# Kernel optimization log

Measured on AMD Instinct MI355X. Metric: run time of the kernel, lower is better.

Reference implementation:

```python
import jax, jax.numpy as jnp
import numpy as np

CLAMP = 15  # relative positions clipped to [-15, 15], shifted to [0, 30]


def setup_inputs() -> dict:
    key = jax.random.key(0)
    ks = jax.random.split(key, 8)
    B, L, C, P = 2, 512, 256, 128
    return {
        "single_repr": jax.random.normal(ks[0], (B, L, C), jnp.float32),
        "pair_bias": jax.random.normal(ks[1], (B, L, L, 2), jnp.float32),
        "mask": jax.random.uniform(ks[2], (B, L), jnp.float32),
        "w_outer": jax.random.normal(ks[3], (C * C, P), jnp.float32) * (1.0 / C),
        "b_outer": jax.random.normal(ks[4], (P,), jnp.float32) * 0.02,
        "pos_embed": jax.random.normal(ks[5], (32, P), jnp.float32) * 0.02,
        "w_bias": jax.random.normal(ks[6], (2, P), jnp.float32) * 0.02,
        "b_bias": jax.random.normal(ks[7], (P,), jnp.float32) * 0.02,
    }


def reference(single_repr, pair_bias, mask, w_outer, b_outer, pos_embed, w_bias, b_bias):
    B, L, C = single_repr.shape
    P = w_outer.shape[-1]
    # Fused outer-product + projection: z[b,i,j,p] = sum_{c,d} s[b,i,c] s[b,j,d] W[c,d,p]
    # done as two matmuls, never materializing the [B,L,L,C,C] tensor.
    W = w_outer.reshape(C, C, P)
    tmp = jnp.einsum('bjd,cdp->bjcp', single_repr, W)          # [B,L,C,P]
    z = jnp.einsum('bic,bjcp->bijp', single_repr, tmp) + b_outer  # [B,L,L,P]
    # pair bias projection (pair_bias_dim=2 != pair_dim -> project)
    z = z + (pair_bias @ w_bias + b_bias)
    # relative-position embedding
    pos = jnp.arange(L)
    rel_pos = jnp.clip(pos[:, None] - pos[None, :], -CLAMP, CLAMP) + CLAMP  # [L,L] in [0,30]
    z = z + pos_embed[rel_pos]
    # pair mask
    pair_mask = mask[:, :, None] * mask[:, None, :]
    z = z * pair_mask[..., None]
    return z
```

## Files before the change

kernel.cpp:

```cpp
#include <hip/hip_runtime.h>
#include <stdint.h>

#define GLOBAL_AS __attribute__((address_space(1)))
#define LDS_AS    __attribute__((address_space(3)))

typedef __attribute__((ext_vector_type(8))) short short8;
typedef __attribute__((ext_vector_type(4))) float f32x4;
typedef __attribute__((ext_vector_type(4))) float float4v;
typedef __attribute__((ext_vector_type(2))) float float2v;
typedef __attribute__((ext_vector_type(4))) unsigned short ushort4v;

static constexpr int Bc = 2;
static constexpr int Lc = 512;
static constexpr int Cc = 256;
static constexpr int Pc = 128;
static constexpr int NP = Pc * Cc;
static constexpr size_t TMPB = (size_t)Lc * NP;

__device__ __forceinline__ unsigned short f2bf(float x) {
  unsigned int u = __builtin_bit_cast(unsigned int, x);
  u += 0x7FFFu + ((u >> 16) & 1u);
  return (unsigned short)(u >> 16);
}

__device__ __forceinline__ void gload_lds16(const void* g, void* l) {
  __builtin_amdgcn_global_load_lds((const GLOBAL_AS unsigned int*)g,
                                   (LDS_AS unsigned int*)l, 16, 0, 0);
}

__global__ void prep_kernel(const float* __restrict__ w,
                            unsigned short* __restrict__ wA,
                            const float* __restrict__ s,
                            unsigned short* __restrict__ s_bf) {
  const int t = threadIdx.x;
  if (blockIdx.x >= 256) {
    const int idx = ((blockIdx.x - 256) * 256 + t) * 4;
    float4v v = *(const float4v*)&s[idx];
    ushort4v o;
    #pragma unroll
    for (int i = 0; i < 4; ++i) o[i] = f2bf(v[i]);
    *(ushort4v*)&s_bf[idx] = o;
    return;
  }
  __shared__ unsigned short lds[128 * 258];
  const int c = blockIdx.x;
  const float* wc = w + (size_t)c * (Cc * Pc);
  #pragma unroll 4
  for (int it = 0; it < 128; ++it) {
    const int idx = it * 256 + t;
    const int d = idx >> 7, p = idx & 127;
    lds[p * 258 + d] = f2bf(wc[idx]);
  }
  __syncthreads();
  #pragma unroll 4
  for (int it = 0; it < 128; ++it) {
    const int idx = it * 256 + t;
    const int p = idx >> 8, d = idx & 255;
    wA[(size_t)p * 65536 + (size_t)c * 256 + d] = lds[p * 258 + d];
  }
}

__device__ __forceinline__ void run_gemm_k256(
    const unsigned short* __restrict__ gA,
    const unsigned short* __restrict__ gB,
    unsigned short (&As)[2][256 * 64],
    unsigned short (&Bs)[2][256 * 64],
    const int tid, const int wave, const int wr, const int wc,
    const int lr, const int lk,
    f32x4 (&acc)[8][4]) {
  auto stage = [&](int sel, int t) {
    const int k0 = t * 64;
    #pragma unroll
    for (int r = 0; r < 4; ++r) {
      const int idx = r * 512 + tid;
      const int row = idx >> 3, col = (idx & 7) << 3;
      gload_lds16(&gA[(size_t)row * 256 + k0 + col],
                  &As[sel][(size_t)(r * 512 + wave * 64) * 8]);
    }
    #pragma unroll
    for (int r = 0; r < 4; ++r) {
      const int idx = r * 512 + tid;
      const int row = idx >> 3, col = (idx & 7) << 3;
      gload_lds16(&gB[(size_t)row * 256 + k0 + col],
                  &Bs[sel][(size_t)(r * 512 + wave * 64) * 8]);
    }
  };

  stage(0, 0);
  __syncthreads();
  #pragma unroll
  for (int t = 0; t < 4; ++t) {
    const int cur = t & 1;
    if (t < 3) stage(cur ^ 1, t + 1);
    #pragma unroll
    for (int kk = 0; kk < 2; ++kk) {
      short8 a[8], b[4];
      #pragma unroll
      for (int m = 0; m < 8; ++m)
        a[m] = *(const short8*)&As[cur][(wr * 128 + m * 16 + lr) * 64 + kk * 32 + lk];
      #pragma unroll
      for (int n = 0; n < 4; ++n)
        b[n] = *(const short8*)&Bs[cur][(wc * 64 + n * 16 + lr) * 64 + kk * 32 + lk];
      #pragma unroll
      for (int m = 0; m < 8; ++m)
        #pragma unroll
        for (int n = 0; n < 4; ++n)
          acc[m][n] = __builtin_amdgcn_mfma_f32_16x16x32_bf16(a[m], b[n], acc[m][n], 0, 0, 0);
    }
    __syncthreads();
  }
}

__global__ __launch_bounds__(512, 2) void gemm1_k(
    const unsigned short* __restrict__ sbf,
    const unsigned short* __restrict__ wA,
    unsigned short* __restrict__ tmpT) {
  __shared__ unsigned short As[2][256 * 64];
  __shared__ unsigned short Bs[2][256 * 64];
  const int tid = threadIdx.x;
  const int wave = tid >> 6, lane = tid & 63;
  const int wr = wave >> 2, wc = wave & 3;
  const int lr = lane & 15, lk = (lane >> 4) << 3;

  const int bid = blockIdx.x;
  const int f = (bid & 7) * 64 + (bid >> 3);
  const int p = f >> 2, nt = f & 3;

  const unsigned short* gA = wA + (size_t)p * 65536;
  const unsigned short* gB = sbf + (size_t)nt * 65536;

  f32x4 acc[8][4];
  const f32x4 zero = {0.f, 0.f, 0.f, 0.f};
  #pragma unroll
  for (int m = 0; m < 8; ++m)
    #pragma unroll
    for (int n = 0; n < 4; ++n) acc[m][n] = zero;

  run_gemm_k256(gA, gB, As, Bs, tid, wave, wr, wc, lr, lk, acc);

  const int cq = wr * 128 + ((lane >> 4) << 2);
  #pragma unroll
  for (int n = 0; n < 4; ++n) {
    const int zj = nt * 256 + wc * 64 + n * 16 + lr;
    unsigned short* dst = tmpT + (size_t)zj * NP + p * 256 + cq;
    #pragma unroll
    for (int m = 0; m < 8; ++m) {
      ushort4v o;
      #pragma unroll
      for (int q = 0; q < 4; ++q) o[q] = f2bf(acc[m][n][q]);
      *(ushort4v*)&dst[m * 16] = o;
    }
  }
}

__global__ __launch_bounds__(512, 2) void gemm2_k(
    const unsigned short* __restrict__ sbf,
    const unsigned short* __restrict__ tmpT,
    const float* __restrict__ pair_bias,
    const float* __restrict__ mask,
    const float* __restrict__ b_outer,
    const float* __restrict__ pos_embed,
    const float* __restrict__ w_bias,
    const float* __restrict__ b_bias,
    float* __restrict__ out) {
  __shared__ unsigned short As[2][256 * 64];
  __shared__ unsigned short Bs[2][256 * 64];
  const int tid = threadIdx.x;
  const int wave = tid >> 6, lane = tid & 63;
  const int wr = wave >> 2, wc = wave & 3;
  const int lr = lane & 15, lk = (lane >> 4) << 3;

  const int bid = blockIdx.x;
  const int f = (bid & 7) * 128 + (bid >> 3);
  const int jt = f >> 1, i0t = f & 1;
  const int z = jt >> 8;

  const unsigned short* gA = tmpT + (size_t)jt * 65536;
  const unsigned short* gB = sbf + (size_t)(z * Lc + i0t * 256) * Cc;

  f32x4 acc[8][4];
  const f32x4 zero = {0.f, 0.f, 0.f, 0.f};
  #pragma unroll
  for (int m = 0; m < 8; ++m)
    #pragma unroll
    for (int n = 0; n < 4; ++n) acc[m][n] = zero;

  run_gemm_k256(gA, gB, As, Bs, tid, wave, wr, wc, lr, lk, acc);

  const int zj = jt * 2 + wr;
  const int j = zj & (Lc - 1);
  const int pq = (lane >> 4) << 2;
  const float mj = mask[z * Lc + j];

  float4v base8[8];
  #pragma unroll
  for (int m = 0; m < 8; ++m) {
    const int pp = m * 16 + pq;
    base8[m] = *(const float4v*)&b_outer[pp] + *(const float4v*)&b_bias[pp];
  }

  #pragma unroll
  for (int n = 0; n < 4; ++n) {
    const int i = i0t * 256 + wc * 64 + n * 16 + lr;
    const float sc = mask[z * Lc + i] * mj;
    const size_t rowoff = ((size_t)(z * Lc + i)) * Lc + j;
    const float2v pb = *(const float2v*)&pair_bias[rowoff * 2];
    int rel = i - j;
    rel = rel < -15 ? -15 : (rel > 15 ? 15 : rel);
    rel += 15;
    const float* pe_row = pos_embed + rel * Pc;
    float* drow = out + rowoff * Pc;
    #pragma unroll
    for (int m = 0; m < 8; ++m) {
      const int pp = m * 16 + pq;
      const float4v wb0 = *(const float4v*)&w_bias[pp];
      const float4v wb1 = *(const float4v*)&w_bias[Pc + pp];
      const float4v pe4 = *(const float4v*)&pe_row[pp];
      float4v v = acc[m][n] + base8[m] + pb[0] * wb0 + pb[1] * wb1 + pe4;
      *(float4v*)&drow[pp] = v * sc;
    }
  }
}

extern "C" void kernel_launch(void* const* d_in, const int* in_sizes, int n_in,
                              void* d_out, int out_size, void* d_ws, size_t ws_size,
                              hipStream_t stream) {
  const float* s         = (const float*)d_in[0];
  const float* pair_bias = (const float*)d_in[1];
  const float* mask      = (const float*)d_in[2];
  const float* w_outer   = (const float*)d_in[3];
  const float* b_outer   = (const float*)d_in[4];
  const float* pos_embed = (const float*)d_in[5];
  const float* w_bias    = (const float*)d_in[6];
  const float* b_bias    = (const float*)d_in[7];
  float* out = (float*)d_out;

  unsigned char* ws = (unsigned char*)d_ws;
  unsigned short* s_bf = (unsigned short*)ws;
  unsigned short* wA   = (unsigned short*)(ws + (512u << 10));
  unsigned short* tmpT = (unsigned short*)(ws + (512u << 10) + (16u << 20));

  prep_kernel<<<512, 256, 0, stream>>>(w_outer, wA, s, s_bf);
  gemm1_k<<<512, 512, 0, stream>>>(s_bf, wA, tmpT);
  gemm2_k<<<1024, 512, 0, stream>>>(s_bf, tmpT, pair_bias, mask,
                                    b_outer, pos_embed, w_bias, b_bias, out);
}
```

Baseline: 435.1 us.

## Swizzle LDS tile layout and use finer-grained waitcnt barriers in GEMM loop

Applies an XOR swizzle to the k-chunk column chosen for each global-to-LDS load, with matching swizzled offsets on the LDS reads, to reduce bank conflicts in the MFMA operand fetches. Replaces __syncthreads with explicit s_waitcnt vmcnt/lgkmcnt plus s_barrier so the prefetch of the next k-tile stays in flight while the current tile is consumed. This relies on hand-counted outstanding loads (vmcnt(8)), which must match the eight loads each stage issues.

```diff
diff --git a/kernel.cpp b/kernel.cpp
--- a/kernel.cpp
+++ b/kernel.cpp
@@ -68,46 +68,65 @@
     const int tid, const int wave, const int wr, const int wc,
     const int lr, const int lk,
     f32x4 (&acc)[8][4]) {
+  const int grow = tid >> 3;
+  const int swz  = ((tid & 7) ^ (grow & 7)) << 3;
+
   auto stage = [&](int sel, int t) {
-    const int k0 = t * 64;
+    const int k0 = t * 64 + swz;
     #pragma unroll
     for (int r = 0; r < 4; ++r) {
-      const int idx = r * 512 + tid;
-      const int row = idx >> 3, col = (idx & 7) << 3;
-      gload_lds16(&gA[(size_t)row * 256 + k0 + col],
+      const int row = r * 64 + grow;
+      gload_lds16(&gA[(size_t)row * 256 + k0],
                   &As[sel][(size_t)(r * 512 + wave * 64) * 8]);
     }
     #pragma unroll
     for (int r = 0; r < 4; ++r) {
-      const int idx = r * 512 + tid;
-      const int row = idx >> 3, col = (idx & 7) << 3;
-      gload_lds16(&gB[(size_t)row * 256 + k0 + col],
+      const int row = r * 64 + grow;
+      gload_lds16(&gB[(size_t)row * 256 + k0],
                   &Bs[sel][(size_t)(r * 512 + wave * 64) * 8]);
     }
   };
 
+  const int hi = lk >> 3;
+  const int xr = lr & 7;
+  const int ro0 = (((0 * 4) + hi) ^ xr) << 3;
+  const int ro1 = (((1 * 4) + hi) ^ xr) << 3;
+
   stage(0, 0);
-  __syncthreads();
+  asm volatile("s_waitcnt vmcnt(0)" ::: "memory");
+  __builtin_amdgcn_s_barrier();
+
   #pragma unroll
   for (int t = 0; t < 4; ++t) {
     const int cur = t & 1;
-    if (t < 3) stage(cur ^ 1, t + 1);
+    if (t < 3) {
+      stage(cur ^ 1, t + 1);
+      asm volatile("s_waitcnt vmcnt(8)" ::: "memory");
+    } else {
+      asm volatile("s_waitcnt vmcnt(0)" ::: "memory");
+    }
+    __builtin_amdgcn_s_barrier();
+    __builtin_amdgcn_sched_barrier(0);
     #pragma unroll
     for (int kk = 0; kk < 2; ++kk) {
+      const int ro = kk ? ro1 : ro0;
       short8 a[8], b[4];
       #pragma unroll
       for (int m = 0; m < 8; ++m)
-        a[m] = *(const short8*)&As[cur][(wr * 128 + m * 16 + lr) * 64 + kk * 32 + lk];
+        a[m] = *(const short8*)&As[cur][(wr * 128 + m * 16 + lr) * 64 + ro];
       #pragma unroll
       for (int n = 0; n < 4; ++n)
-        b[n] = *(const short8*)&Bs[cur][(wc * 64 + n * 16 + lr) * 64 + kk * 32 + lk];
+        b[n] = *(const short8*)&Bs[cur][(wc * 64 + n * 16 + lr) * 64 + ro];
       #pragma unroll
       for (int m = 0; m < 8; ++m)
         #pragma unroll
         for (int n = 0; n < 4; ++n)
           acc[m][n] = __builtin_amdgcn_mfma_f32_16x16x32_bf16(a[m], b[n], acc[m][n], 0, 0, 0);
     }
-    __syncthreads();
+    if (t < 3) {
+      asm volatile("s_waitcnt lgkmcnt(0)" ::: "memory");
+      __builtin_amdgcn_s_barrier();
+    }
   }
 }
 
```

Result: slower. 455.3 us (+4.6%).

## Shrink GEMM tiles to 128x128 with 256 threads and single-buffered LDS

Applied to the files above, without the earlier changes.

Both GEMM kernels move from 256x256 tiles with 512 threads and double-buffered LDS to 128x128 tiles with 256 threads, a single LDS buffer and a non-unrolled K loop. This quadruples the block count, cuts LDS per block from 128KB to 32KB and halves the accumulator registers, aiming for more resident blocks and better latency hiding across CUs. The cost is lower operand reuse per block, more global traffic, and no overlap of loads with MFMA inside a block. The epilogue also hoists the w_bias loads out of the row loop.

```diff
diff --git a/kernel.cpp b/kernel.cpp
--- a/kernel.cpp
+++ b/kernel.cpp
@@ -60,91 +60,85 @@
   }
 }
 
-__device__ __forceinline__ void run_gemm_k256(
+__device__ __forceinline__ void run_gemm128_k256(
     const unsigned short* __restrict__ gA,
     const unsigned short* __restrict__ gB,
-    unsigned short (&As)[2][256 * 64],
-    unsigned short (&Bs)[2][256 * 64],
-    const int tid, const int wave, const int wr, const int wc,
+    unsigned short (&As)[128 * 64],
+    unsigned short (&Bs)[128 * 64],
+    const int tid, const int wave, const int wr, const int wcn,
     const int lr, const int lk,
-    f32x4 (&acc)[8][4]) {
-  auto stage = [&](int sel, int t) {
-    const int k0 = t * 64;
-    #pragma unroll
-    for (int r = 0; r < 4; ++r) {
-      const int idx = r * 512 + tid;
+    f32x4 (&acc)[4][4]) {
+  #pragma unroll 1
+  for (int kt = 0; kt < 4; ++kt) {
+    const int k0 = kt * 64;
+    __syncthreads();
+    #pragma unroll
+    for (int op = 0; op < 4; ++op) {
+      const int idx = op * 256 + tid;
       const int row = idx >> 3, col = (idx & 7) << 3;
       gload_lds16(&gA[(size_t)row * 256 + k0 + col],
-                  &As[sel][(size_t)(r * 512 + wave * 64) * 8]);
-    }
-    #pragma unroll
-    for (int r = 0; r < 4; ++r) {
-      const int idx = r * 512 + tid;
+                  &As[(size_t)(op * 256 + wave * 64) * 8]);
+    }
+    #pragma unroll
+    for (int op = 0; op < 4; ++op) {
+      const int idx = op * 256 + tid;
       const int row = idx >> 3, col = (idx & 7) << 3;
       gload_lds16(&gB[(size_t)row * 256 + k0 + col],
-                  &Bs[sel][(size_t)(r * 512 + wave * 64) * 8]);
-    }
-  };
-
-  stage(0, 0);
-  __syncthreads();
-  #pragma unroll
-  for (int t = 0; t < 4; ++t) {
-    const int cur = t & 1;
-    if (t < 3) stage(cur ^ 1, t + 1);
+                  &Bs[(size_t)(op * 256 + wave * 64) * 8]);
+    }
+    __syncthreads();
     #pragma unroll
     for (int kk = 0; kk < 2; ++kk) {
-      short8 a[8], b[4];
-      #pragma unroll
-      for (int m = 0; m < 8; ++m)
-        a[m] = *(const short8*)&As[cur][(wr * 128 + m * 16 + lr) * 64 + kk * 32 + lk];
+      short8 a[4], b[4];
+      #pragma unroll
+      for (int m = 0; m < 4; ++m)
+        a[m] = *(const short8*)&As[(wr * 64 + m * 16 + lr) * 64 + kk * 32 + lk];
       #pragma unroll
       for (int n = 0; n < 4; ++n)
-        b[n] = *(const short8*)&Bs[cur][(wc * 64 + n * 16 + lr) * 64 + kk * 32 + lk];
-      #pragma unroll
-      for (int m = 0; m < 8; ++m)
+        b[n] = *(const short8*)&Bs[(wcn * 64 + n * 16 + lr) * 64 + kk * 32 + lk];
+      #pragma unroll
+      for (int m = 0; m < 4; ++m)
         #pragma unroll
         for (int n = 0; n < 4; ++n)
           acc[m][n] = __builtin_amdgcn_mfma_f32_16x16x32_bf16(a[m], b[n], acc[m][n], 0, 0, 0);
     }
-    __syncthreads();
-  }
-}
-
-__global__ __launch_bounds__(512, 2) void gemm1_k(
+  }
+}
+
+__global__ __launch_bounds__(256) void gemm1_k(
     const unsigned short* __restrict__ sbf,
     const unsigned short* __restrict__ wA,
     unsigned short* __restrict__ tmpT) {
-  __shared__ unsigned short As[2][256 * 64];
-  __shared__ unsigned short Bs[2][256 * 64];
+  __shared__ unsigned short As[128 * 64];
+  __shared__ unsigned short Bs[128 * 64];
   const int tid = threadIdx.x;
   const int wave = tid >> 6, lane = tid & 63;
-  const int wr = wave >> 2, wc = wave & 3;
+  const int wr = wave >> 1, wcn = wave & 1;
   const int lr = lane & 15, lk = (lane >> 4) << 3;
 
   const int bid = blockIdx.x;
-  const int f = (bid & 7) * 64 + (bid >> 3);
-  const int p = f >> 2, nt = f & 3;
-
-  const unsigned short* gA = wA + (size_t)p * 65536;
-  const unsigned short* gB = sbf + (size_t)nt * 65536;
-
-  f32x4 acc[8][4];
+  const int f = (bid & 7) * 256 + (bid >> 3);
+  const int mt = f >> 3, nt = f & 7;
+
+  const unsigned short* gA = wA + (size_t)mt * 32768;
+  const unsigned short* gB = sbf + (size_t)nt * 128 * 256;
+
+  f32x4 acc[4][4];
   const f32x4 zero = {0.f, 0.f, 0.f, 0.f};
   #pragma unroll
-  for (int m = 0; m < 8; ++m)
+  for (int m = 0; m < 4; ++m)
     #pragma unroll
     for (int n = 0; n < 4; ++n) acc[m][n] = zero;
 
-  run_gemm_k256(gA, gB, As, Bs, tid, wave, wr, wc, lr, lk, acc);
-
-  const int cq = wr * 128 + ((lane >> 4) << 2);
+  run_gemm128_k256(gA, gB, As, Bs, tid, wave, wr, wcn, lr, lk, acc);
+
+  const int rbase = wr * 64 + ((lane >> 4) << 2);
   #pragma unroll
   for (int n = 0; n < 4; ++n) {
-    const int zj = nt * 256 + wc * 64 + n * 16 + lr;
-    unsigned short* dst = tmpT + (size_t)zj * NP + p * 256 + cq;
-    #pragma unroll
-    for (int m = 0; m < 8; ++m) {
+    const int zj = nt * 128 + wcn * 64 + n * 16 + lr;
+    unsigned short* dst = tmpT + (size_t)zj * NP + mt * 128 + rbase;
+    #pragma unroll
+    for (int m = 0; m < 4; ++m) {
       ushort4v o;
       #pragma unroll
       for (int q = 0; q < 4; ++q) o[q] = f2bf(acc[m][n][q]);
@@ -153,7 +147,7 @@
   }
 }
 
-__global__ __launch_bounds__(512, 2) void gemm2_k(
+__global__ __launch_bounds__(256) void gemm2_k(
     const unsigned short* __restrict__ sbf,
     const unsigned short* __restrict__ tmpT,
     const float* __restrict__ pair_bias,
@@ -163,45 +157,46 @@
     const float* __restrict__ w_bias,
     const float* __restrict__ b_bias,
     float* __restrict__ out) {
-  __shared__ unsigned short As[2][256 * 64];
-  __shared__ unsigned short Bs[2][256 * 64];
+  __shared__ unsigned short As[128 * 64];
+  __shared__ unsigned short Bs[128 * 64];
   const int tid = threadIdx.x;
   const int wave = tid >> 6, lane = tid & 63;
-  const int wr = wave >> 2, wc = wave & 3;
+  const int wr = wave >> 1, wcn = wave & 1;
   const int lr = lane & 15, lk = (lane >> 4) << 3;
 
   const int bid = blockIdx.x;
-  const int f = (bid & 7) * 128 + (bid >> 3);
-  const int jt = f >> 1, i0t = f & 1;
-  const int z = jt >> 8;
-
-  const unsigned short* gA = tmpT + (size_t)jt * 65536;
-  const unsigned short* gB = sbf + (size_t)(z * Lc + i0t * 256) * Cc;
-
-  f32x4 acc[8][4];
+  const int f = (bid & 7) * 512 + (bid >> 3);
+  const int zj = f >> 2, nt = f & 3;
+  const int z = zj >> 9;
+  const int j = zj & (Lc - 1);
+
+  const unsigned short* gA = tmpT + (size_t)zj * NP;
+  const unsigned short* gB = sbf + ((size_t)(z * Lc) + nt * 128) * Cc;
+
+  f32x4 acc[4][4];
   const f32x4 zero = {0.f, 0.f, 0.f, 0.f};
   #pragma unroll
-  for (int m = 0; m < 8; ++m)
+  for (int m = 0; m < 4; ++m)
     #pragma unroll
     for (int n = 0; n < 4; ++n) acc[m][n] = zero;
 
-  run_gemm_k256(gA, gB, As, Bs, tid, wave, wr, wc, lr, lk, acc);
-
-  const int zj = jt * 2 + wr;
-  const int j = zj & (Lc - 1);
-  const int pq = (lane >> 4) << 2;
+  run_gemm128_k256(gA, gB, As, Bs, tid, wave, wr, wcn, lr, lk, acc);
+
+  const int pbase = wr * 64 + ((lane >> 4) << 2);
   const float mj = mask[z * Lc + j];
 
-  float4v base8[8];
-  #pragma unroll
-  for (int m = 0; m < 8; ++m) {
-    const int pp = m * 16 + pq;
-    base8[m] = *(const float4v*)&b_outer[pp] + *(const float4v*)&b_bias[pp];
+  float4v base4[4], wb0v[4], wb1v[4];
+  #pragma unroll
+  for (int m = 0; m < 4; ++m) {
+    const int pp = pbase + m * 16;
+    base4[m] = *(const float4v*)&b_outer[pp] + *(const float4v*)&b_bias[pp];
+    wb0v[m] = *(const float4v*)&w_bias[pp];
+    wb1v[m] = *(const float4v*)&w_bias[Pc + pp];
   }
 
   #pragma unroll
   for (int n = 0; n < 4; ++n) {
-    const int i = i0t * 256 + wc * 64 + n * 16 + lr;
+    const int i = nt * 128 + wcn * 64 + n * 16 + lr;
     const float sc = mask[z * Lc + i] * mj;
     const size_t rowoff = ((size_t)(z * Lc + i)) * Lc + j;
     const float2v pb = *(const float2v*)&pair_bias[rowoff * 2];
@@ -211,12 +206,10 @@
     const float* pe_row = pos_embed + rel * Pc;
     float* drow = out + rowoff * Pc;
     #pragma unroll
-    for (int m = 0; m < 8; ++m) {
-      const int pp = m * 16 + pq;
-      const float4v wb0 = *(const float4v*)&w_bias[pp];
-      const float4v wb1 = *(const float4v*)&w_bias[Pc + pp];
+    for (int m = 0; m < 4; ++m) {
+      const int pp = pbase + m * 16;
       const float4v pe4 = *(const float4v*)&pe_row[pp];
-      float4v v = acc[m][n] + base8[m] + pb[0] * wb0 + pb[1] * wb1 + pe4;
+      float4v v = acc[m][n] + base4[m] + pb[0] * wb0v[m] + pb[1] * wb1v[m] + pe4;
       *(float4v*)&drow[pp] = v * sc;
     }
   }
@@ -241,7 +234,7 @@
   unsigned short* tmpT = (unsigned short*)(ws + (512u << 10) + (16u << 20));
 
   prep_kernel<<<512, 256, 0, stream>>>(w_outer, wA, s, s_bf);
-  gemm1_k<<<512, 512, 0, stream>>>(s_bf, wA, tmpT);
-  gemm2_k<<<1024, 512, 0, stream>>>(s_bf, tmpT, pair_bias, mask,
+  gemm1_k<<<2048, 256, 0, stream>>>(s_bf, wA, tmpT);
+  gemm2_k<<<4096, 256, 0, stream>>>(s_bf, tmpT, pair_bias, mask,
                                     b_outer, pos_embed, w_bias, b_bias, out);
 }
```

Result: no change. 427.9 us (-1.7%).
